# Kernel tuning notes

Measured on AMD Instinct MI355X. Metric: run time of the kernel, lower is better.

The kernel has to match this reference:

```python
import jax, jax.numpy as jnp
import numpy as np

N, F_IN, HEADS, D_HEAD, HID, OUT, E = 50000, 128, 4, 64, 256, 2, 800000
NEG_SLOPE = 0.2


def setup_inputs() -> dict:
    key = jax.random.key(0)
    ks = jax.random.split(key, 12)
    x = jax.random.normal(ks[0], (N, F_IN), dtype=jnp.float32)
    edge_index = jax.random.randint(ks[1], (2, E), 0, N, dtype=jnp.int64)
    s = 0.05
    W_gat = jax.random.normal(ks[2], (F_IN, HEADS * D_HEAD), dtype=jnp.float32) * s
    att_src = jax.random.normal(ks[3], (HEADS, D_HEAD), dtype=jnp.float32) * s
    att_dst = jax.random.normal(ks[4], (HEADS, D_HEAD), dtype=jnp.float32) * s
    b_gat = jnp.zeros((HEADS * D_HEAD,), dtype=jnp.float32)
    W1 = jax.random.normal(ks[5], (HEADS * D_HEAD, HID), dtype=jnp.float32) * s
    b1 = jnp.zeros((HID,), dtype=jnp.float32)
    W2 = jax.random.normal(ks[6], (HID, HID), dtype=jnp.float32) * s
    b2 = jnp.zeros((HID,), dtype=jnp.float32)
    W3 = jax.random.normal(ks[7], (HID, OUT), dtype=jnp.float32) * s
    b3 = jnp.zeros((OUT,), dtype=jnp.float32)
    return {"x": x, "edge_index": edge_index, "W_gat": W_gat, "att_src": att_src,
            "att_dst": att_dst, "b_gat": b_gat, "W1": W1, "b1": b1,
            "W2": W2, "b2": b2, "W3": W3, "b3": b3}


def _gat(x, edge_index, W_gat, att_src, att_dst, b_gat):
    n = x.shape[0]
    loop = jnp.arange(n, dtype=edge_index.dtype)
    src = jnp.concatenate([edge_index[0], loop])  # [E+N] message sources j
    dst = jnp.concatenate([edge_index[1], loop])  # [E+N] message targets i
    h = (x @ W_gat).reshape(n, HEADS, D_HEAD)      # [N,H,D]
    a_s = jnp.einsum('nhd,hd->nh', h, att_src)     # [N,H]
    a_d = jnp.einsum('nhd,hd->nh', h, att_dst)     # [N,H]
    e = a_s[src] + a_d[dst]                        # [E',H]
    e = jax.nn.leaky_relu(e, NEG_SLOPE)
    # per-destination-node softmax over incoming edges (numerically stable)
    emax = jax.ops.segment_max(e, dst, num_segments=n)
    e = jnp.exp(e - emax[dst])
    denom = jax.ops.segment_sum(e, dst, num_segments=n)
    alpha = e / denom[dst]                         # [E',H]
    msg = h[src] * alpha[:, :, None]               # [E',H,D]
    out = jax.ops.segment_sum(msg, dst, num_segments=n)  # [N,H,D]
    return out.reshape(n, HEADS * D_HEAD) + b_gat


def reference(x, edge_index, W_gat, att_src, att_dst, b_gat, W1, b1, W2, b2, W3, b3):
    h = _gat(x, edge_index, W_gat, att_src, att_dst, b_gat)
    h = jax.nn.relu(h @ W1 + b1)
    h = jax.nn.relu(h @ W2 + b2)
    return h @ W3 + b3
```

## Files before the change

### kernel.cpp

```cpp
#include <hip/hip_runtime.h>
#include <math.h>

#define N_NODES 50000
#define NP 50048
#define F_IN 128
#define HD 256
#define HID 256
#define NE 800000
#define CAP 64
#define NEG_SLOPE 0.2f

typedef __attribute__((ext_vector_type(8))) __bf16 bf16x8;
typedef __attribute__((ext_vector_type(4))) __bf16 bf16x4;
typedef __attribute__((ext_vector_type(4))) float f32x4;

#define GLD_LDS16(g, l)                                                      \
    __builtin_amdgcn_global_load_lds(                                        \
        (const __attribute__((address_space(1))) unsigned int*)(g),          \
        (__attribute__((address_space(3))) unsigned int*)(l), 16, 0, 0)

#define PB_CONV 6250
#define PB_INIT 196
#define PB_WG   128
#define PB_W1   256
#define PB_W2   256

__global__ __launch_bounds__(256) void prep_kernel(const float* __restrict__ x,
                                                   const float* __restrict__ Wg,
                                                   const float* __restrict__ W1,
                                                   const float* __restrict__ W2,
                                                   __bf16* __restrict__ xb,
                                                   __bf16* __restrict__ Wg_t,
                                                   __bf16* __restrict__ W1_t,
                                                   __bf16* __restrict__ W2_t,
                                                   int* __restrict__ cnt,
                                                   int* __restrict__ bucket) {
    int b = blockIdx.x, t = threadIdx.x;
    if (b < PB_CONV) {
        int i = b * 256 + t;
        float4 v = ((const float4*)x)[i];
        bf16x4 o = {(__bf16)v.x, (__bf16)v.y, (__bf16)v.z, (__bf16)v.w};
        ((bf16x4*)xb)[i] = o;
    } else if (b < PB_CONV + PB_INIT) {
        int n = (b - PB_CONV) * 256 + t;
        if (n < N_NODES) { cnt[n] = 1; bucket[n * CAP] = n; }
    } else if (b < PB_CONV + PB_INIT + PB_WG) {
        int i = (b - PB_CONV - PB_INIT) * 256 + t;
        int m = i >> 7, k = i & 127;
        Wg_t[i] = (__bf16)Wg[(size_t)k * HD + m];
    } else if (b < PB_CONV + PB_INIT + PB_WG + PB_W1) {
        int i = (b - PB_CONV - PB_INIT - PB_WG) * 256 + t;
        int m = i >> 8, k = i & 255;
        W1_t[i] = (__bf16)W1[(size_t)k * HID + m];
    } else {
        int i = (b - PB_CONV - PB_INIT - PB_WG - PB_W1) * 256 + t;
        int m = i >> 8, k = i & 255;
        W2_t[i] = (__bf16)W2[(size_t)k * HID + m];
    }
}

__global__ __launch_bounds__(256) void fill_kernel(const int* __restrict__ ew,
                                                   int* cnt, int* bucket) {
    int e = blockIdx.x * 256 + threadIdx.x;
    int hi = ew[2 * e + 1];
    unsigned long long bal = __ballot(hi != 0);
    int src, dst;
    if (bal == 0) { src = ew[2 * e]; dst = ew[2 * NE + 2 * e]; }
    else          { src = ew[e];     dst = ew[NE + e]; }
    int pos = atomicAdd(&cnt[dst], 1);
    if (pos < CAP) bucket[dst * CAP + pos] = src;
}

__global__ __launch_bounds__(256) void gemm1_attn_kernel(const __bf16* __restrict__ A,
                                                         const __bf16* __restrict__ Bt,
                                                         const float* __restrict__ att_src,
                                                         const float* __restrict__ att_dst,
                                                         __bf16* __restrict__ h,
                                                         float* __restrict__ a_s,
                                                         float* __restrict__ a_d) {
    __shared__ __bf16 As[64 * 32];
    __shared__ __bf16 Bs[256 * 32];
    const int t = threadIdx.x;
    const int lane = t & 63, wv = t >> 6;
    const int lr = lane & 15, q = lane >> 4, lk = q * 8;
    const int col_off = wv * 64;
    const int row0 = blockIdx.x * 64;
    const int sr = t >> 2, sk = (t & 3) * 8;

    f32x4 acc[4][4];
#pragma unroll
    for (int r = 0; r < 4; ++r)
#pragma unroll
        for (int c = 0; c < 4; ++c) acc[r][c] = f32x4{0.f, 0.f, 0.f, 0.f};

    for (int k0 = 0; k0 < F_IN; k0 += 32) {
        GLD_LDS16(&A[(size_t)(row0 + sr) * F_IN + k0 + sk], &As[sr * 32 + sk]);
#pragma unroll
        for (int s = 0; s < 4; ++s) {
            int r = s * 64 + sr;
            GLD_LDS16(&Bt[(size_t)r * F_IN + k0 + sk], &Bs[r * 32 + sk]);
        }
        __syncthreads();
        bf16x8 af[4], bfr[4];
#pragma unroll
        for (int i = 0; i < 4; ++i) {
            af[i]  = *(const bf16x8*)&As[(i * 16 + lr) * 32 + lk];
            bfr[i] = *(const bf16x8*)&Bs[(col_off + i * 16 + lr) * 32 + lk];
        }
#pragma unroll
        for (int r = 0; r < 4; ++r)
#pragma unroll
            for (int c = 0; c < 4; ++c)
                acc[r][c] = __builtin_amdgcn_mfma_f32_16x16x32_bf16(af[r], bfr[c], acc[r][c], 0, 0, 0);
        __syncthreads();
    }

    float asv[4], adv[4];
#pragma unroll
    for (int c = 0; c < 4; ++c) {
        int col = col_off + c * 16 + lr;
        asv[c] = att_src[col];
        adv[c] = att_dst[col];
    }
    float ps[4][4], pd[4][4];
#pragma unroll
    for (int r = 0; r < 4; ++r)
#pragma unroll
        for (int i = 0; i < 4; ++i) { ps[r][i] = 0.f; pd[r][i] = 0.f; }

#pragma unroll
    for (int c = 0; c < 4; ++c) {
        int col = col_off + c * 16 + lr;
#pragma unroll
        for (int r = 0; r < 4; ++r) {
#pragma unroll
            for (int i = 0; i < 4; ++i) {
                int row = row0 + r * 16 + q * 4 + i;
                float v = acc[r][c][i];
                h[(size_t)row * HD + col] = (__bf16)v;
                ps[r][i] += v * asv[c];
                pd[r][i] += v * adv[c];
            }
        }
    }
#pragma unroll
    for (int r = 0; r < 4; ++r)
#pragma unroll
        for (int i = 0; i < 4; ++i) {
#pragma unroll
            for (int m = 1; m < 16; m <<= 1) {
                ps[r][i] += __shfl_xor(ps[r][i], m);
                pd[r][i] += __shfl_xor(pd[r][i], m);
            }
        }
    if (lr == 0) {
#pragma unroll
        for (int r = 0; r < 4; ++r)
#pragma unroll
            for (int i = 0; i < 4; ++i) {
                int row = row0 + r * 16 + q * 4 + i;
                a_s[row * 4 + wv] = ps[r][i];
                a_d[row * 4 + wv] = pd[r][i];
            }
    }
}

__device__ __forceinline__ float lrelu(float v) { return v >= 0.f ? v : NEG_SLOPE * v; }

__global__ __launch_bounds__(256) void gat_aggregate_kernel(const __bf16* __restrict__ h,
                                                            const float* __restrict__ a_s,
                                                            const float* __restrict__ a_d,
                                                            const int* __restrict__ cnt,
                                                            const int* __restrict__ bucket,
                                                            const float* __restrict__ b_gat,
                                                            __bf16* __restrict__ gat) {
    __shared__ int s_src[4][64];
    __shared__ float s_alpha[4][64][4];
    int lane = threadIdx.x & 63;
    int wv = threadIdx.x >> 6;
    int n = blockIdx.x * 4 + wv;

    int deg = cnt[n];
    if (deg > CAP) deg = CAP;
    int src = -1;
    float4 e = {-1e30f, -1e30f, -1e30f, -1e30f};
    float4 ad = *(const float4*)&a_d[n * 4];
    if (lane < deg) {
        src = bucket[n * CAP + lane];
        float4 as4 = *(const float4*)&a_s[src * 4];
        e.x = lrelu(as4.x + ad.x);
        e.y = lrelu(as4.y + ad.y);
        e.z = lrelu(as4.z + ad.z);
        e.w = lrelu(as4.w + ad.w);
    }
    float4 m = e;
#pragma unroll
    for (int off = 1; off < 64; off <<= 1) {
        m.x = fmaxf(m.x, __shfl_xor(m.x, off));
        m.y = fmaxf(m.y, __shfl_xor(m.y, off));
        m.z = fmaxf(m.z, __shfl_xor(m.z, off));
        m.w = fmaxf(m.w, __shfl_xor(m.w, off));
    }
    float4 wgt = {0, 0, 0, 0};
    if (lane < deg) {
        wgt.x = __expf(e.x - m.x); wgt.y = __expf(e.y - m.y);
        wgt.z = __expf(e.z - m.z); wgt.w = __expf(e.w - m.w);
    }
    float4 s = wgt;
#pragma unroll
    for (int off = 1; off < 64; off <<= 1) {
        s.x += __shfl_xor(s.x, off); s.y += __shfl_xor(s.y, off);
        s.z += __shfl_xor(s.z, off); s.w += __shfl_xor(s.w, off);
    }
    float4 alpha;
    alpha.x = wgt.x / s.x; alpha.y = wgt.y / s.y;
    alpha.z = wgt.z / s.z; alpha.w = wgt.w / s.w;

    s_src[wv][lane] = src;
    *(float4*)&s_alpha[wv][lane][0] = alpha;
    __syncthreads();

    int head = lane >> 4;
    float ax = 0.f, ay = 0.f, az = 0.f, aw = 0.f;
    int j = 0;
    for (; j + 4 <= deg; j += 4) {
        int s0 = s_src[wv][j], s1 = s_src[wv][j + 1];
        int s2 = s_src[wv][j + 2], s3 = s_src[wv][j + 3];
        float a0 = s_alpha[wv][j][head],     a1 = s_alpha[wv][j + 1][head];
        float a2 = s_alpha[wv][j + 2][head], a3 = s_alpha[wv][j + 3][head];
        bf16x4 h0 = *(const bf16x4*)&h[(size_t)s0 * HD + lane * 4];
        bf16x4 h1 = *(const bf16x4*)&h[(size_t)s1 * HD + lane * 4];
        bf16x4 h2 = *(const bf16x4*)&h[(size_t)s2 * HD + lane * 4];
        bf16x4 h3 = *(const bf16x4*)&h[(size_t)s3 * HD + lane * 4];
        ax += a0 * (float)h0.x + a1 * (float)h1.x + a2 * (float)h2.x + a3 * (float)h3.x;
        ay += a0 * (float)h0.y + a1 * (float)h1.y + a2 * (float)h2.y + a3 * (float)h3.y;
        az += a0 * (float)h0.z + a1 * (float)h1.z + a2 * (float)h2.z + a3 * (float)h3.z;
        aw += a0 * (float)h0.w + a1 * (float)h1.w + a2 * (float)h2.w + a3 * (float)h3.w;
    }
    for (; j < deg; ++j) {
        int sj = s_src[wv][j];
        float aj = s_alpha[wv][j][head];
        bf16x4 hv = *(const bf16x4*)&h[(size_t)sj * HD + lane * 4];
        ax += aj * (float)hv.x; ay += aj * (float)hv.y;
        az += aj * (float)hv.z; aw += aj * (float)hv.w;
    }
    float4 bg = *(const float4*)&b_gat[lane * 4];
    bf16x4 o = {(__bf16)(ax + bg.x), (__bf16)(ay + bg.y),
                (__bf16)(az + bg.z), (__bf16)(aw + bg.w)};
    *(bf16x4*)&gat[(size_t)n * HD + lane * 4] = o;
}

__global__ __launch_bounds__(256) void fused_mlp_kernel(const __bf16* __restrict__ A,
                                                        const __bf16* __restrict__ W1t,
                                                        const __bf16* __restrict__ W2t,
                                                        const float* __restrict__ b1,
                                                        const float* __restrict__ b2,
                                                        const float* __restrict__ W3,
                                                        const float* __restrict__ b3,
                                                        float* __restrict__ out) {
    __shared__ __bf16 As[64 * 32];
    __shared__ __bf16 Ws[256 * 32];
    __shared__ __bf16 h1s[8 * 64 * 32];
    __shared__ float s_out[64][2];
    const int t = threadIdx.x;
    const int lane = t & 63, wv = t >> 6;
    const int lr = lane & 15, q = lane >> 4, lk = q * 8;
    const int col_off = wv * 64;
    const int row0 = blockIdx.x * 64;
    const int sr = t >> 2, sk = (t & 3) * 8;

    if (t < 128) ((float*)s_out)[t] = 0.f;

    f32x4 acc[4][4];
#pragma unroll
    for (int r = 0; r < 4; ++r)
#pragma unroll
        for (int c = 0; c < 4; ++c) acc[r][c] = f32x4{0.f, 0.f, 0.f, 0.f};

    for (int k0 = 0; k0 < HD; k0 += 32) {
        GLD_LDS16(&A[(size_t)(row0 + sr) * HD + k0 + sk], &As[sr * 32 + sk]);
#pragma unroll
        for (int s = 0; s < 4; ++s) {
            int r = s * 64 + sr;
            GLD_LDS16(&W1t[(size_t)r * HD + k0 + sk], &Ws[r * 32 + sk]);
        }
        __syncthreads();
        bf16x8 af[4], bfr[4];
#pragma unroll
        for (int i = 0; i < 4; ++i) {
            af[i]  = *(const bf16x8*)&As[(i * 16 + lr) * 32 + lk];
            bfr[i] = *(const bf16x8*)&Ws[(col_off + i * 16 + lr) * 32 + lk];
        }
#pragma unroll
        for (int r = 0; r < 4; ++r)
#pragma unroll
            for (int c = 0; c < 4; ++c)
                acc[r][c] = __builtin_amdgcn_mfma_f32_16x16x32_bf16(af[r], bfr[c], acc[r][c], 0, 0, 0);
        __syncthreads();
    }
#pragma unroll
    for (int c = 0; c < 4; ++c) {
        int col = col_off + c * 16 + lr;
        float bv = b1[col];
        int cb = (col >> 5) * 2048;
        int kk = col & 31;
#pragma unroll
        for (int r = 0; r < 4; ++r)
#pragma unroll
            for (int i = 0; i < 4; ++i) {
                int row = r * 16 + q * 4 + i;
                float v = fmaxf(acc[r][c][i] + bv, 0.f);
                h1s[cb + row * 32 + kk] = (__bf16)v;
                acc[r][c][i] = 0.f;
            }
    }
    __syncthreads();

    for (int k0 = 0; k0 < HID; k0 += 32) {
#pragma unroll
        for (int s = 0; s < 4; ++s) {
            int r = s * 64 + sr;
            GLD_LDS16(&W2t[(size_t)r * HID + k0 + sk], &Ws[r * 32 + sk]);
        }
        __syncthreads();
        const int cb = (k0 >> 5) * 2048;
        bf16x8 af[4], bfr[4];
#pragma unroll
        for (int i = 0; i < 4; ++i) {
            af[i]  = *(const bf16x8*)&h1s[cb + (i * 16 + lr) * 32 + lk];
            bfr[i] = *(const bf16x8*)&Ws[(col_off + i * 16 + lr) * 32 + lk];
        }
#pragma unroll
        for (int r = 0; r < 4; ++r)
#pragma unroll
            for (int c = 0; c < 4; ++c)
                acc[r][c] = __builtin_amdgcn_mfma_f32_16x16x32_bf16(af[r], bfr[c], acc[r][c], 0, 0, 0);
        __syncthreads();
    }

    float b2v[4], w30[4], w31[4];
#pragma unroll
    for (int c = 0; c < 4; ++c) {
        int col = col_off + c * 16 + lr;
        b2v[c] = b2[col];
        w30[c] = W3[col * 2];
        w31[c] = W3[col * 2 + 1];
    }
#pragma unroll
    for (int r = 0; r < 4; ++r) {
#pragma unroll
        for (int i = 0; i < 4; ++i) {
            float o0 = 0.f, o1 = 0.f;
#pragma unroll
            for (int c = 0; c < 4; ++c) {
                float v = fmaxf(acc[r][c][i] + b2v[c], 0.f);
                o0 += v * w30[c];
                o1 += v * w31[c];
            }
#pragma unroll
            for (int m = 1; m < 16; m <<= 1) {
                o0 += __shfl_xor(o0, m);
                o1 += __shfl_xor(o1, m);
            }
            if (lr == 0) {
                int row = r * 16 + q * 4 + i;
                atomicAdd(&s_out[row][0], o0);
                atomicAdd(&s_out[row][1], o1);
            }
        }
    }
    __syncthreads();
    if (t < 128) {
        int row = t >> 1, o = t & 1;
        int g = row0 + row;
        if (g < N_NODES) out[g * 2 + o] = s_out[row][o] + b3[o];
    }
}

extern "C" void kernel_launch(void* const* d_in, const int* in_sizes, int n_in,
                              void* d_out, int out_size, void* d_ws, size_t ws_size,
                              hipStream_t stream) {
    const float* x       = (const float*)d_in[0];
    const int*   ei      = (const int*)d_in[1];
    const float* W_gat   = (const float*)d_in[2];
    const float* att_src = (const float*)d_in[3];
    const float* att_dst = (const float*)d_in[4];
    const float* b_gat   = (const float*)d_in[5];
    const float* W1      = (const float*)d_in[6];
    const float* b1      = (const float*)d_in[7];
    const float* W2      = (const float*)d_in[8];
    const float* b2      = (const float*)d_in[9];
    const float* W3      = (const float*)d_in[10];
    const float* b3      = (const float*)d_in[11];
    float* out = (float*)d_out;

    char* ws = (char*)d_ws;
    __bf16* x_bf   = (__bf16*)ws;  ws += (size_t)NP * F_IN * 2;
    __bf16* h_bf   = (__bf16*)ws;  ws += (size_t)NP * HD * 2;
    __bf16* gat_bf = (__bf16*)ws;  ws += (size_t)NP * HD * 2;
    __bf16* Wg_t   = (__bf16*)ws;  ws += (size_t)HD * F_IN * 2;
    __bf16* W1_t   = (__bf16*)ws;  ws += (size_t)HID * HD * 2;
    __bf16* W2_t   = (__bf16*)ws;  ws += (size_t)HID * HID * 2;
    float* a_s     = (float*)ws;   ws += (size_t)NP * 4 * 4;
    float* a_d     = (float*)ws;   ws += (size_t)NP * 4 * 4;
    int* cnt       = (int*)ws;     ws += (size_t)N_NODES * 4;
    int* bucket    = (int*)ws;     ws += (size_t)N_NODES * CAP * 4;

    prep_kernel<<<PB_CONV + PB_INIT + PB_WG + PB_W1 + PB_W2, 256, 0, stream>>>(
        x, W_gat, W1, W2, x_bf, Wg_t, W1_t, W2_t, cnt, bucket);
    fill_kernel<<<NE / 256, 256, 0, stream>>>(ei, cnt, bucket);
    gemm1_attn_kernel<<<NP / 64, 256, 0, stream>>>(x_bf, Wg_t, att_src, att_dst,
                                                   h_bf, a_s, a_d);
    gat_aggregate_kernel<<<N_NODES / 4, 256, 0, stream>>>(h_bf, a_s, a_d, cnt, bucket,
                                                          b_gat, gat_bf);
    fused_mlp_kernel<<<NP / 64, 256, 0, stream>>>(gat_bf, W1_t, W2_t, b1, b2, W3, b3, out);
}
```

Baseline: 257.8 us.

## Split GAT aggregation into softmax pass and XCD-sliced column gather kernel

Splits the fused softmax+aggregate kernel into two kernels. The first writes per-edge fp16 alpha to a head-major buffer. The second gathers h one 32-column slice at a time, with the slice chosen by blockIdx&7, presumably so each XCD's L2 only caches its own column slice of h. The fill kernel is also replicated 8x, each copy handling only the destination-node slice for its XCD, so the atomics and bucket writes stay L2-local. The bucket shrinks to 16-bit source indices. The costs are extra launches, 8x redundant reads of edge_index, an extra alpha buffer round trip, and reduced alpha precision.

After: 304.0 us. 1.18x slower.

```diff
diff --git a/kernel.cpp b/kernel.cpp
--- a/kernel.cpp
+++ b/kernel.cpp
@@ -9,10 +9,13 @@
 #define NE 800000
 #define CAP 64
 #define NEG_SLOPE 0.2f
+#define NS (N_NODES * 64)
+#define DST_SLICE 6250
 
 typedef __attribute__((ext_vector_type(8))) __bf16 bf16x8;
 typedef __attribute__((ext_vector_type(4))) __bf16 bf16x4;
 typedef __attribute__((ext_vector_type(4))) float f32x4;
+typedef __attribute__((ext_vector_type(8))) unsigned short u16x8;
 
 #define GLD_LDS16(g, l)                                                      \
     __builtin_amdgcn_global_load_lds(                                        \
@@ -34,7 +37,7 @@
                                                    __bf16* __restrict__ W1_t,
                                                    __bf16* __restrict__ W2_t,
                                                    int* __restrict__ cnt,
-                                                   int* __restrict__ bucket) {
+                                                   unsigned short* __restrict__ bucket) {
     int b = blockIdx.x, t = threadIdx.x;
     if (b < PB_CONV) {
         int i = b * 256 + t;
@@ -43,7 +46,7 @@
         ((bf16x4*)xb)[i] = o;
     } else if (b < PB_CONV + PB_INIT) {
         int n = (b - PB_CONV) * 256 + t;
-        if (n < N_NODES) { cnt[n] = 1; bucket[n * CAP] = n; }
+        if (n < N_NODES) { cnt[n] = 1; bucket[n * CAP] = (unsigned short)n; }
     } else if (b < PB_CONV + PB_INIT + PB_WG) {
         int i = (b - PB_CONV - PB_INIT) * 256 + t;
         int m = i >> 7, k = i & 127;
@@ -60,15 +63,21 @@
 }
 
 __global__ __launch_bounds__(256) void fill_kernel(const int* __restrict__ ew,
-                                                   int* cnt, int* bucket) {
-    int e = blockIdx.x * 256 + threadIdx.x;
+                                                   int* cnt,
+                                                   unsigned short* __restrict__ bucket) {
+    int b = blockIdx.x;
+    int xcd = b & 7, chunk = b >> 3;
+    int e = chunk * 256 + threadIdx.x;
     int hi = ew[2 * e + 1];
     unsigned long long bal = __ballot(hi != 0);
     int src, dst;
     if (bal == 0) { src = ew[2 * e]; dst = ew[2 * NE + 2 * e]; }
     else          { src = ew[e];     dst = ew[NE + e]; }
-    int pos = atomicAdd(&cnt[dst], 1);
-    if (pos < CAP) bucket[dst * CAP + pos] = src;
+    int lo = xcd * DST_SLICE;
+    if (dst >= lo && dst < lo + DST_SLICE) {
+        int pos = atomicAdd(&cnt[dst], 1);
+        if (pos < CAP) bucket[dst * CAP + pos] = (unsigned short)src;
+    }
 }
 
 __global__ __launch_bounds__(256) void gemm1_attn_kernel(const __bf16* __restrict__ A,
@@ -167,26 +176,21 @@
 
 __device__ __forceinline__ float lrelu(float v) { return v >= 0.f ? v : NEG_SLOPE * v; }
 
-__global__ __launch_bounds__(256) void gat_aggregate_kernel(const __bf16* __restrict__ h,
-                                                            const float* __restrict__ a_s,
-                                                            const float* __restrict__ a_d,
-                                                            const int* __restrict__ cnt,
-                                                            const int* __restrict__ bucket,
-                                                            const float* __restrict__ b_gat,
-                                                            __bf16* __restrict__ gat) {
-    __shared__ int s_src[4][64];
-    __shared__ float s_alpha[4][64][4];
+__global__ __launch_bounds__(256) void attn_softmax_kernel(const float* __restrict__ a_s,
+                                                           const float* __restrict__ a_d,
+                                                           const int* __restrict__ cnt,
+                                                           const unsigned short* __restrict__ bucket,
+                                                           _Float16* __restrict__ alpha_out) {
     int lane = threadIdx.x & 63;
     int wv = threadIdx.x >> 6;
     int n = blockIdx.x * 4 + wv;
 
     int deg = cnt[n];
     if (deg > CAP) deg = CAP;
-    int src = -1;
     float4 e = {-1e30f, -1e30f, -1e30f, -1e30f};
     float4 ad = *(const float4*)&a_d[n * 4];
     if (lane < deg) {
-        src = bucket[n * CAP + lane];
+        int src = bucket[n * CAP + lane];
         float4 as4 = *(const float4*)&a_s[src * 4];
         e.x = lrelu(as4.x + ad.x);
         e.y = lrelu(as4.y + ad.y);
@@ -212,42 +216,72 @@
         s.x += __shfl_xor(s.x, off); s.y += __shfl_xor(s.y, off);
         s.z += __shfl_xor(s.z, off); s.w += __shfl_xor(s.w, off);
     }
-    float4 alpha;
-    alpha.x = wgt.x / s.x; alpha.y = wgt.y / s.y;
-    alpha.z = wgt.z / s.z; alpha.w = wgt.w / s.w;
-
-    s_src[wv][lane] = src;
-    *(float4*)&s_alpha[wv][lane][0] = alpha;
+    int base = n * 64 + lane;
+    alpha_out[0 * NS + base] = (_Float16)(wgt.x / s.x);
+    alpha_out[1 * NS + base] = (_Float16)(wgt.y / s.y);
+    alpha_out[2 * NS + base] = (_Float16)(wgt.z / s.z);
+    alpha_out[3 * NS + base] = (_Float16)(wgt.w / s.w);
+}
+
+__global__ __launch_bounds__(256) void gather_kernel(const __bf16* __restrict__ h,
+                                                     const _Float16* __restrict__ alpha,
+                                                     const int* __restrict__ cnt,
+                                                     const unsigned short* __restrict__ bucket,
+                                                     const float* __restrict__ b_gat,
+                                                     __bf16* __restrict__ gat) {
+    __shared__ unsigned short s_src[32 * 64];
+    __shared__ _Float16 s_al[32 * 64];
+    __shared__ int s_deg[32];
+    const int b = blockIdx.x;
+    const int slice = b & 7;
+    const int n0 = (b >> 3) * 32;
+    const int head = slice >> 1;
+    const int t = threadIdx.x;
+
+    {
+        int node = t >> 3;
+        int off = (t & 7) * 8;
+        if (n0 + node < N_NODES) {
+            *(u16x8*)&s_src[node * 64 + off] =
+                *(const u16x8*)&bucket[(size_t)(n0 + node) * 64 + off];
+            *(u16x8*)&s_al[node * 64 + off] =
+                *(const u16x8*)&alpha[(size_t)head * NS + (size_t)(n0 + node) * 64 + off];
+        }
+        if (t < 32) {
+            int n = n0 + t;
+            int d = (n < N_NODES) ? cnt[n] : 0;
+            s_deg[t] = d > CAP ? CAP : d;
+        }
+    }
     __syncthreads();
 
-    int head = lane >> 4;
+    const int lane = t & 63, wv = t >> 6;
+    const int g = lane >> 3;
+    const int node = wv * 8 + g;
+    const int cidx = (lane & 7) * 4;
+    const int n = n0 + node;
+    const int deg = s_deg[node];
+    int md = deg;
+#pragma unroll
+    for (int off = 8; off < 64; off <<= 1) md = max(md, __shfl_xor(md, off));
+
+    const __bf16* hsl = h + slice * 32 + cidx;
     float ax = 0.f, ay = 0.f, az = 0.f, aw = 0.f;
-    int j = 0;
-    for (; j + 4 <= deg; j += 4) {
-        int s0 = s_src[wv][j], s1 = s_src[wv][j + 1];
-        int s2 = s_src[wv][j + 2], s3 = s_src[wv][j + 3];
-        float a0 = s_alpha[wv][j][head],     a1 = s_alpha[wv][j + 1][head];
-        float a2 = s_alpha[wv][j + 2][head], a3 = s_alpha[wv][j + 3][head];
-        bf16x4 h0 = *(const bf16x4*)&h[(size_t)s0 * HD + lane * 4];
-        bf16x4 h1 = *(const bf16x4*)&h[(size_t)s1 * HD + lane * 4];
-        bf16x4 h2 = *(const bf16x4*)&h[(size_t)s2 * HD + lane * 4];
-        bf16x4 h3 = *(const bf16x4*)&h[(size_t)s3 * HD + lane * 4];
-        ax += a0 * (float)h0.x + a1 * (float)h1.x + a2 * (float)h2.x + a3 * (float)h3.x;
-        ay += a0 * (float)h0.y + a1 * (float)h1.y + a2 * (float)h2.y + a3 * (float)h3.y;
-        az += a0 * (float)h0.z + a1 * (float)h1.z + a2 * (float)h2.z + a3 * (float)h3.z;
-        aw += a0 * (float)h0.w + a1 * (float)h1.w + a2 * (float)h2.w + a3 * (float)h3.w;
-    }
-    for (; j < deg; ++j) {
-        int sj = s_src[wv][j];
-        float aj = s_alpha[wv][j][head];
-        bf16x4 hv = *(const bf16x4*)&h[(size_t)sj * HD + lane * 4];
-        ax += aj * (float)hv.x; ay += aj * (float)hv.y;
-        az += aj * (float)hv.z; aw += aj * (float)hv.w;
-    }
-    float4 bg = *(const float4*)&b_gat[lane * 4];
-    bf16x4 o = {(__bf16)(ax + bg.x), (__bf16)(ay + bg.y),
-                (__bf16)(az + bg.z), (__bf16)(aw + bg.w)};
-    *(bf16x4*)&gat[(size_t)n * HD + lane * 4] = o;
+    for (int j = 0; j < md; ++j) {
+        int sj = s_src[node * 64 + j];
+        float aj = (float)s_al[node * 64 + j];
+        if (j < deg) {
+            bf16x4 hv = *(const bf16x4*)&hsl[sj << 8];
+            ax += aj * (float)hv.x; ay += aj * (float)hv.y;
+            az += aj * (float)hv.z; aw += aj * (float)hv.w;
+        }
+    }
+    if (n < N_NODES) {
+        float4 bg = *(const float4*)&b_gat[slice * 32 + cidx];
+        bf16x4 o = {(__bf16)(ax + bg.x), (__bf16)(ay + bg.y),
+                    (__bf16)(az + bg.z), (__bf16)(aw + bg.w)};
+        *(bf16x4*)&gat[(size_t)n * HD + slice * 32 + cidx] = o;
+    }
 }
 
 __global__ __launch_bounds__(256) void fused_mlp_kernel(const __bf16* __restrict__ A,
@@ -403,15 +437,18 @@
     __bf16* W2_t   = (__bf16*)ws;  ws += (size_t)HID * HID * 2;
     float* a_s     = (float*)ws;   ws += (size_t)NP * 4 * 4;
     float* a_d     = (float*)ws;   ws += (size_t)NP * 4 * 4;
+    _Float16* alp  = (_Float16*)ws; ws += (size_t)4 * NS * 2;
     int* cnt       = (int*)ws;     ws += (size_t)N_NODES * 4;
-    int* bucket    = (int*)ws;     ws += (size_t)N_NODES * CAP * 4;
+    unsigned short* bucket = (unsigned short*)ws;
+    ws += (size_t)N_NODES * CAP * 2;
 
     prep_kernel<<<PB_CONV + PB_INIT + PB_WG + PB_W1 + PB_W2, 256, 0, stream>>>(
         x, W_gat, W1, W2, x_bf, Wg_t, W1_t, W2_t, cnt, bucket);
-    fill_kernel<<<NE / 256, 256, 0, stream>>>(ei, cnt, bucket);
+    fill_kernel<<<(NE / 256) * 8, 256, 0, stream>>>(ei, cnt, bucket);
     gemm1_attn_kernel<<<NP / 64, 256, 0, stream>>>(x_bf, Wg_t, att_src, att_dst,
                                                    h_bf, a_s, a_d);
-    gat_aggregate_kernel<<<N_NODES / 4, 256, 0, stream>>>(h_bf, a_s, a_d, cnt, bucket,
-                                                          b_gat, gat_bf);
+    attn_softmax_kernel<<<N_NODES / 4, 256, 0, stream>>>(a_s, a_d, cnt, bucket, alp);
+    gather_kernel<<<((N_NODES + 31) / 32) * 8, 256, 0, stream>>>(h_bf, alp, cnt, bucket,
+                                                                 b_gat, gat_bf);
     fused_mlp_kernel<<<NP / 64, 256, 0, stream>>>(gat_bf, W1_t, W2_t, b1, b2, W3, b3, out);
 }
```

## Fuse x bf16 conversion into GEMM, use 16-bit buckets, widen aggregation loads

Applied to the files above, without the earlier changes.

Removes the separate x-to-bf16 pass: the GEMM now loads fp32 x directly, converts it in registers and stores it to LDS, with bounds masking for padded rows. Edge buckets are stored as 16-bit indices to halve adjacency traffic. The aggregation kernel now splits each wave into two halves that each process alternate edges with 16-byte bf16x8 loads, then combines the halves with a cross-lane shuffle. The 16-bit bucket cannot represent node ids above 65535, which holds only because N is 50000.

Result: no change. 253.5 us (-1.7%).

```diff
diff --git a/kernel.cpp b/kernel.cpp
--- a/kernel.cpp
+++ b/kernel.cpp
@@ -19,48 +19,41 @@
         (const __attribute__((address_space(1))) unsigned int*)(g),          \
         (__attribute__((address_space(3))) unsigned int*)(l), 16, 0, 0)
 
-#define PB_CONV 6250
 #define PB_INIT 196
 #define PB_WG   128
 #define PB_W1   256
 #define PB_W2   256
 
-__global__ __launch_bounds__(256) void prep_kernel(const float* __restrict__ x,
-                                                   const float* __restrict__ Wg,
+__global__ __launch_bounds__(256) void prep_kernel(const float* __restrict__ Wg,
                                                    const float* __restrict__ W1,
                                                    const float* __restrict__ W2,
-                                                   __bf16* __restrict__ xb,
                                                    __bf16* __restrict__ Wg_t,
                                                    __bf16* __restrict__ W1_t,
                                                    __bf16* __restrict__ W2_t,
                                                    int* __restrict__ cnt,
-                                                   int* __restrict__ bucket) {
+                                                   unsigned short* __restrict__ bucket) {
     int b = blockIdx.x, t = threadIdx.x;
-    if (b < PB_CONV) {
-        int i = b * 256 + t;
-        float4 v = ((const float4*)x)[i];
-        bf16x4 o = {(__bf16)v.x, (__bf16)v.y, (__bf16)v.z, (__bf16)v.w};
-        ((bf16x4*)xb)[i] = o;
-    } else if (b < PB_CONV + PB_INIT) {
-        int n = (b - PB_CONV) * 256 + t;
-        if (n < N_NODES) { cnt[n] = 1; bucket[n * CAP] = n; }
-    } else if (b < PB_CONV + PB_INIT + PB_WG) {
-        int i = (b - PB_CONV - PB_INIT) * 256 + t;
+    if (b < PB_INIT) {
+        int n = b * 256 + t;
+        if (n < N_NODES) { cnt[n] = 1; bucket[n * CAP] = (unsigned short)n; }
+    } else if (b < PB_INIT + PB_WG) {
+        int i = (b - PB_INIT) * 256 + t;
         int m = i >> 7, k = i & 127;
         Wg_t[i] = (__bf16)Wg[(size_t)k * HD + m];
-    } else if (b < PB_CONV + PB_INIT + PB_WG + PB_W1) {
-        int i = (b - PB_CONV - PB_INIT - PB_WG) * 256 + t;
+    } else if (b < PB_INIT + PB_WG + PB_W1) {
+        int i = (b - PB_INIT - PB_WG) * 256 + t;
         int m = i >> 8, k = i & 255;
         W1_t[i] = (__bf16)W1[(size_t)k * HID + m];
     } else {
-        int i = (b - PB_CONV - PB_INIT - PB_WG - PB_W1) * 256 + t;
+        int i = (b - PB_INIT - PB_WG - PB_W1) * 256 + t;
         int m = i >> 8, k = i & 255;
         W2_t[i] = (__bf16)W2[(size_t)k * HID + m];
     }
 }
 
 __global__ __launch_bounds__(256) void fill_kernel(const int* __restrict__ ew,
-                                                   int* cnt, int* bucket) {
+                                                   int* cnt,
+                                                   unsigned short* __restrict__ bucket) {
     int e = blockIdx.x * 256 + threadIdx.x;
     int hi = ew[2 * e + 1];
     unsigned long long bal = __ballot(hi != 0);
@@ -68,10 +61,10 @@
     if (bal == 0) { src = ew[2 * e]; dst = ew[2 * NE + 2 * e]; }
     else          { src = ew[e];     dst = ew[NE + e]; }
     int pos = atomicAdd(&cnt[dst], 1);
-    if (pos < CAP) bucket[dst * CAP + pos] = src;
-}
-
-__global__ __launch_bounds__(256) void gemm1_attn_kernel(const __bf16* __restrict__ A,
+    if (pos < CAP) bucket[dst * CAP + pos] = (unsigned short)src;
+}
+
+__global__ __launch_bounds__(256) void gemm1_attn_kernel(const float* __restrict__ x,
                                                          const __bf16* __restrict__ Bt,
                                                          const float* __restrict__ att_src,
                                                          const float* __restrict__ att_dst,
@@ -86,6 +79,8 @@
     const int col_off = wv * 64;
     const int row0 = blockIdx.x * 64;
     const int sr = t >> 2, sk = (t & 3) * 8;
+    const int arow = row0 + sr;
+    const bool avalid = arow < N_NODES;
 
     f32x4 acc[4][4];
 #pragma unroll
@@ -94,7 +89,16 @@
         for (int c = 0; c < 4; ++c) acc[r][c] = f32x4{0.f, 0.f, 0.f, 0.f};
 
     for (int k0 = 0; k0 < F_IN; k0 += 32) {
-        GLD_LDS16(&A[(size_t)(row0 + sr) * F_IN + k0 + sk], &As[sr * 32 + sk]);
+        float4 v0 = {0, 0, 0, 0}, v1 = {0, 0, 0, 0};
+        if (avalid) {
+            const float* xp = &x[(size_t)arow * F_IN + k0 + sk];
+            v0 = *(const float4*)xp;
+            v1 = *(const float4*)(xp + 4);
+        }
+        bf16x8 o;
+        o[0] = (__bf16)v0.x; o[1] = (__bf16)v0.y; o[2] = (__bf16)v0.z; o[3] = (__bf16)v0.w;
+        o[4] = (__bf16)v1.x; o[5] = (__bf16)v1.y; o[6] = (__bf16)v1.z; o[7] = (__bf16)v1.w;
+        *(bf16x8*)&As[sr * 32 + sk] = o;
 #pragma unroll
         for (int s = 0; s < 4; ++s) {
             int r = s * 64 + sr;
@@ -171,10 +175,10 @@
                                                             const float* __restrict__ a_s,
                                                             const float* __restrict__ a_d,
                                                             const int* __restrict__ cnt,
-                                                            const int* __restrict__ bucket,
+                                                            const unsigned short* __restrict__ bucket,
                                                             const float* __restrict__ b_gat,
                                                             __bf16* __restrict__ gat) {
-    __shared__ int s_src[4][64];
+    __shared__ unsigned short s_src[4][64];
     __shared__ float s_alpha[4][64][4];
     int lane = threadIdx.x & 63;
     int wv = threadIdx.x >> 6;
@@ -182,7 +186,7 @@
 
     int deg = cnt[n];
     if (deg > CAP) deg = CAP;
-    int src = -1;
+    int src = n;
     float4 e = {-1e30f, -1e30f, -1e30f, -1e30f};
     float4 ad = *(const float4*)&a_d[n * 4];
     if (lane < deg) {
@@ -212,42 +216,55 @@
         s.x += __shfl_xor(s.x, off); s.y += __shfl_xor(s.y, off);
         s.z += __shfl_xor(s.z, off); s.w += __shfl_xor(s.w, off);
     }
-    float4 alpha;
-    alpha.x = wgt.x / s.x; alpha.y = wgt.y / s.y;
-    alpha.z = wgt.z / s.z; alpha.w = wgt.w / s.w;
-
-    s_src[wv][lane] = src;
-    *(float4*)&s_alpha[wv][lane][0] = alpha;
+    s_src[wv][lane] = (unsigned short)src;
+    s_alpha[wv][lane][0] = wgt.x / s.x;
+    s_alpha[wv][lane][1] = wgt.y / s.y;
+    s_alpha[wv][lane][2] = wgt.z / s.z;
+    s_alpha[wv][lane][3] = wgt.w / s.w;
     __syncthreads();
 
-    int head = lane >> 4;
-    float ax = 0.f, ay = 0.f, az = 0.f, aw = 0.f;
+    const int half = lane >> 5;
+    const int l32 = lane & 31;
+    const int c0 = l32 * 8;
+    const int head = l32 >> 3;
+    float acc[8];
+#pragma unroll
+    for (int k = 0; k < 8; ++k) acc[k] = 0.f;
+
+    const int mde = (deg + 1) & ~1;
     int j = 0;
-    for (; j + 4 <= deg; j += 4) {
-        int s0 = s_src[wv][j], s1 = s_src[wv][j + 1];
-        int s2 = s_src[wv][j + 2], s3 = s_src[wv][j + 3];
-        float a0 = s_alpha[wv][j][head],     a1 = s_alpha[wv][j + 1][head];
-        float a2 = s_alpha[wv][j + 2][head], a3 = s_alpha[wv][j + 3][head];
-        bf16x4 h0 = *(const bf16x4*)&h[(size_t)s0 * HD + lane * 4];
-        bf16x4 h1 = *(const bf16x4*)&h[(size_t)s1 * HD + lane * 4];
-        bf16x4 h2 = *(const bf16x4*)&h[(size_t)s2 * HD + lane * 4];
-        bf16x4 h3 = *(const bf16x4*)&h[(size_t)s3 * HD + lane * 4];
-        ax += a0 * (float)h0.x + a1 * (float)h1.x + a2 * (float)h2.x + a3 * (float)h3.x;
-        ay += a0 * (float)h0.y + a1 * (float)h1.y + a2 * (float)h2.y + a3 * (float)h3.y;
-        az += a0 * (float)h0.z + a1 * (float)h1.z + a2 * (float)h2.z + a3 * (float)h3.z;
-        aw += a0 * (float)h0.w + a1 * (float)h1.w + a2 * (float)h2.w + a3 * (float)h3.w;
-    }
-    for (; j < deg; ++j) {
-        int sj = s_src[wv][j];
-        float aj = s_alpha[wv][j][head];
-        bf16x4 hv = *(const bf16x4*)&h[(size_t)sj * HD + lane * 4];
-        ax += aj * (float)hv.x; ay += aj * (float)hv.y;
-        az += aj * (float)hv.z; aw += aj * (float)hv.w;
-    }
-    float4 bg = *(const float4*)&b_gat[lane * 4];
-    bf16x4 o = {(__bf16)(ax + bg.x), (__bf16)(ay + bg.y),
-                (__bf16)(az + bg.z), (__bf16)(aw + bg.w)};
-    *(bf16x4*)&gat[(size_t)n * HD + lane * 4] = o;
+    for (; j + 4 <= mde; j += 4) {
+        int j0 = j + half, j1 = j + 2 + half;
+        int s0 = s_src[wv][j0], s1 = s_src[wv][j1];
+        float a0 = s_alpha[wv][j0][head], a1 = s_alpha[wv][j1][head];
+        bf16x8 h0 = *(const bf16x8*)&h[(size_t)s0 * HD + c0];
+        bf16x8 h1 = *(const bf16x8*)&h[(size_t)s1 * HD + c0];
+#pragma unroll
+        for (int k = 0; k < 8; ++k)
+            acc[k] += a0 * (float)h0[k] + a1 * (float)h1[k];
+    }
+    for (; j < mde; j += 2) {
+        int j0 = j + half;
+        int s0 = s_src[wv][j0];
+        float a0 = s_alpha[wv][j0][head];
+        bf16x8 h0 = *(const bf16x8*)&h[(size_t)s0 * HD + c0];
+#pragma unroll
+        for (int k = 0; k < 8; ++k)
+            acc[k] += a0 * (float)h0[k];
+    }
+#pragma unroll
+    for (int k = 0; k < 8; ++k) acc[k] += __shfl_xor(acc[k], 32);
+
+    if (half == 0) {
+        float4 bg0 = *(const float4*)&b_gat[c0];
+        float4 bg1 = *(const float4*)&b_gat[c0 + 4];
+        bf16x8 o;
+        o[0] = (__bf16)(acc[0] + bg0.x); o[1] = (__bf16)(acc[1] + bg0.y);
+        o[2] = (__bf16)(acc[2] + bg0.z); o[3] = (__bf16)(acc[3] + bg0.w);
+        o[4] = (__bf16)(acc[4] + bg1.x); o[5] = (__bf16)(acc[5] + bg1.y);
+        o[6] = (__bf16)(acc[6] + bg1.z); o[7] = (__bf16)(acc[7] + bg1.w);
+        *(bf16x8*)&gat[(size_t)n * HD + c0] = o;
+    }
 }
 
 __global__ __launch_bounds__(256) void fused_mlp_kernel(const __bf16* __restrict__ A,
@@ -395,7 +412,6 @@
     float* out = (float*)d_out;
 
     char* ws = (char*)d_ws;
-    __bf16* x_bf   = (__bf16*)ws;  ws += (size_t)NP * F_IN * 2;
     __bf16* h_bf   = (__bf16*)ws;  ws += (size_t)NP * HD * 2;
     __bf16* gat_bf = (__bf16*)ws;  ws += (size_t)NP * HD * 2;
     __bf16* Wg_t   = (__bf16*)ws;  ws += (size_t)HD * F_IN * 2;
@@ -404,12 +420,13 @@
     float* a_s     = (float*)ws;   ws += (size_t)NP * 4 * 4;
     float* a_d     = (float*)ws;   ws += (size_t)NP * 4 * 4;
     int* cnt       = (int*)ws;     ws += (size_t)N_NODES * 4;
-    int* bucket    = (int*)ws;     ws += (size_t)N_NODES * CAP * 4;
-
-    prep_kernel<<<PB_CONV + PB_INIT + PB_WG + PB_W1 + PB_W2, 256, 0, stream>>>(
-        x, W_gat, W1, W2, x_bf, Wg_t, W1_t, W2_t, cnt, bucket);
+    unsigned short* bucket = (unsigned short*)ws;
+    ws += (size_t)N_NODES * CAP * 2;
+
+    prep_kernel<<<PB_INIT + PB_WG + PB_W1 + PB_W2, 256, 0, stream>>>(
+        W_gat, W1, W2, Wg_t, W1_t, W2_t, cnt, bucket);
     fill_kernel<<<NE / 256, 256, 0, stream>>>(ei, cnt, bucket);
-    gemm1_attn_kernel<<<NP / 64, 256, 0, stream>>>(x_bf, Wg_t, att_src, att_dst,
+    gemm1_attn_kernel<<<NP / 64, 256, 0, stream>>>(x, Wg_t, att_src, att_dst,
                                                    h_bf, a_s, a_d);
     gat_aggregate_kernel<<<N_NODES / 4, 256, 0, stream>>>(h_bf, a_s, a_d, cnt, bucket,
                                                           b_gat, gat_bf);
```
